# Kernel tuning notes

Measured on AMD Instinct MI355X. Metric: run time of the kernel, lower is better.

Reference implementation:

```python
import jax, jax.numpy as jnp
import numpy as np

N1, N2 = 8192, 4096
NUM_ITERS = 8  # bounded version of the data-dependent while-loop in Revision_PRED
EPS = 1e-6


def _make_boxes(key, n):
    k1, k2 = jax.random.split(key)
    lt = jax.random.uniform(k1, (n, 2), minval=0.0, maxval=800.0)
    wh = jax.random.uniform(k2, (n, 2), minval=1.0, maxval=200.0)
    return jnp.concatenate([lt, lt + wh], axis=1)  # valid xyxy boxes


def setup_inputs() -> dict:
    key = jax.random.key(0)
    ks = jax.random.split(key, 6)
    return {
        "bboxes1": _make_boxes(ks[0], N1),
        "scores1": jax.random.uniform(ks[1], (N1,)),
        "classes1": jax.random.randint(ks[2], (N1,), 0, 80),
        "bboxes2": _make_boxes(ks[3], N2),
        "scores2": jax.random.uniform(ks[4], (N2,)),
        "classes2": jax.random.randint(ks[5], (N2,), 0, 80),
    }


def bbox_overlaps_iou(b1, b2, eps=EPS):
    # b1: [N1,4], b2: [N2,4] xyxy -> [N1,N2] IoU (mode='iou', is_aligned=False)
    area1 = (b1[:, 2] - b1[:, 0]) * (b1[:, 3] - b1[:, 1])
    area2 = (b2[:, 2] - b2[:, 0]) * (b2[:, 3] - b2[:, 1])
    lt = jnp.maximum(b1[:, None, :2], b2[None, :, :2])
    rb = jnp.minimum(b1[:, None, 2:], b2[None, :, 2:])
    wh = jnp.clip(rb - lt, 0.0)
    overlap = wh[..., 0] * wh[..., 1]
    union = jnp.maximum(area1[:, None] + area2[None, :] - overlap, eps)
    return overlap / union


def reference(bboxes1, scores1, classes1, bboxes2, scores2, classes2):
    # Faithful JAX version of Revision_PRED: pairwise IoU + iterative
    # suppression (index_put_ of 0.5) + scatter of winning predictions.
    ious = bbox_overlaps_iou(bboxes1, bboxes2)
    cols = jnp.arange(ious.shape[1])

    def body(ious, _):
        refine_gt = (ious > 0.5).any(axis=0)            # [N2]
        refine_inds = jnp.argmax(ious, axis=0)          # [N2] best pred per box2
        need_refine = scores1[refine_inds] >= scores2
        lower = refine_gt & (~need_refine)              # == (~refine_gt|~need_refine)&refine_gt
        # index_put_ of 0.5 at (refine_inds[lower], lower cols); no-op elsewhere
        new_vals = jnp.where(lower, 0.5, ious[refine_inds, cols])
        ious = ious.at[refine_inds, cols].set(new_vals)
        return ious, None

    # Bounded, idempotent-once-converged replacement for the `while True` loop.
    ious, _ = jax.lax.scan(body, ious, None, length=NUM_ITERS)

    refine_gt = (ious > 0.5).any(axis=0)
    refine_inds = jnp.argmax(ious, axis=0)
    b2 = jnp.where(refine_gt[:, None], bboxes1[refine_inds], bboxes2)
    s2 = jnp.where(refine_gt, scores1[refine_inds], scores2)
    c2 = jnp.where(refine_gt, classes1[refine_inds], classes2)
    refined_boxes = (b2 + jnp.abs(b2)) * 0.5            # clamp negatives to 0
    missing_mask = (ious < 0.5).all(axis=1)             # preds kept as 'missing'
    return refined_boxes, s2, c2, missing_mask, ious
```

## Files before the change

### kernel.cpp

```cpp
#include <hip/hip_runtime.h>


constexpr int TOPK = 9;

__device__ __forceinline__ void key_insert(unsigned long long (&t)[TOPK],
                                           unsigned long long pk) {
    if (pk > t[TOPK - 1]) {
#pragma unroll
        for (int j = TOPK - 1; j >= 0; --j) {
            const bool gt_cur  = pk > t[j];
            const bool gt_prev = (j > 0) ? (pk > t[j - 1]) : false;
            if (gt_cur) t[j] = gt_prev ? t[j - 1] : pk;
        }
    }
}

__global__ __launch_bounds__(256) void iou_cand_kernel(
    const float* __restrict__ b1, const float* __restrict__ b2,
    float* __restrict__ ious,
    unsigned int* __restrict__ cnt, unsigned long long* __restrict__ cand,
    unsigned char* __restrict__ rowflag,
    int n1, int n2, int rps, int cap)
{
    const int tid = blockIdx.x * blockDim.x + threadIdx.x;
    const int c0 = tid * 4;
    if (c0 >= n2) return;
    const int r0 = blockIdx.y * rps;
    const int r1 = min(r0 + rps, n1);

    float4 bx[4]; float ar[4];
#pragma unroll
    for (int k = 0; k < 4; ++k) {
        bx[k] = reinterpret_cast<const float4*>(b2)[c0 + k];
        ar[k] = __fmul_rn(__fsub_rn(bx[k].z, bx[k].x),
                          __fsub_rn(bx[k].w, bx[k].y));
    }

    float* orow = ious + (size_t)r0 * n2 + c0;
    for (int r = r0; r < r1; ++r, orow += n2) {
        const float4 p = reinterpret_cast<const float4*>(b1)[r];
        const float a1 = __fmul_rn(__fsub_rn(p.z, p.x), __fsub_rn(p.w, p.y));
        float v[4], ovs[4], uns[4];
#pragma unroll
        for (int k = 0; k < 4; ++k) {
            const float wx = fmaxf(__fsub_rn(fminf(p.z, bx[k].z),
                                             fmaxf(p.x, bx[k].x)), 0.0f);
            const float wy = fmaxf(__fsub_rn(fminf(p.w, bx[k].w),
                                             fmaxf(p.y, bx[k].y)), 0.0f);
            const float ov = __fmul_rn(wx, wy);
            const float un = fmaxf(__fsub_rn(__fadd_rn(a1, ar[k]), ov), 1e-6f);
            ovs[k] = ov; uns[k] = un;
            float rc = __builtin_amdgcn_rcpf(un);
            rc = rc * fmaf(-un, rc, 2.0f);
            v[k] = ov * rc;
        }

        const float vmax = fmaxf(fmaxf(v[0], v[1]), fmaxf(v[2], v[3]));
        if (vmax > 0.499999f) {
#pragma unroll
            for (int k = 0; k < 4; ++k) {
                if (v[k] > 0.499999f) {
                    const float ve = __fdiv_rn(ovs[k], uns[k]);
                    v[k] = ve;
                    if (ve >= 0.5f) {
                        rowflag[r] = 1;
                        if (ve > 0.5f) {
                            const unsigned int idx = atomicAdd(&cnt[c0 + k], 1u);
                            if (idx < (unsigned int)cap)
                                cand[(size_t)idx * n2 + (c0 + k)] =
                                    ((unsigned long long)__float_as_uint(ve) << 32)
                                  | (unsigned long long)(~(unsigned int)r);
                        }
                    }
                }
            }
        }
        *reinterpret_cast<float4*>(orow) = make_float4(v[0], v[1], v[2], v[3]);
    }
}

__global__ __launch_bounds__(64) void refine_missing_kernel(
    const float* __restrict__ b1, const float* __restrict__ s1,
    const int* __restrict__ c1,
    const float* __restrict__ b2, const float* __restrict__ s2,
    const int* __restrict__ c2,
    const unsigned int* __restrict__ cnt,
    const unsigned long long* __restrict__ cand,
    const unsigned char* __restrict__ rowflag,
    float* __restrict__ out_boxes, float* __restrict__ out_s,
    float* __restrict__ out_c, float* __restrict__ out_m,
    float* __restrict__ ious,
    int n1, int n2, int cap)
{
    const int tid = blockIdx.x * blockDim.x + threadIdx.x;

    if (tid < n1)
        out_m[tid] = rowflag[tid] ? 0.0f : 1.0f;

    const int c = tid;
    if (c >= n2) return;

    unsigned long long t[TOPK];
#pragma unroll
    for (int j = 0; j < TOPK; ++j) t[j] = 0ull;

    const int n = (int)cnt[c];
    if (n <= cap) {
        const unsigned long long* L = cand + c;
        for (int e = 0; e < n; ++e)
            key_insert(t, L[(size_t)e * n2]);
    } else {
        for (int r = 0; r < n1; ++r) {
            const float v = ious[(size_t)r * n2 + c];
            if (v > 0.5f)
                key_insert(t, ((unsigned long long)__float_as_uint(v) << 32)
                            | (unsigned long long)(~(unsigned int)r));
        }
    }

    int m = 0;
#pragma unroll
    for (int j = 0; j < TOPK; ++j) m += (t[j] != 0ull) ? 1 : 0;

    int   ti[TOPK];
    float s1v[TOPK];
    const float s2c = s2[c];
#pragma unroll
    for (int j = 0; j < TOPK; ++j) {
        ti[j]  = (int)~(unsigned int)(t[j] & 0xffffffffull);
        s1v[j] = (j < m) ? s1[ti[j]] : 0.0f;
    }

    int k = 0;
#pragma unroll
    for (int j = 0; j < 8; ++j)
        if (j < m && k == j && s1v[j] < s2c) k = j + 1;

#pragma unroll
    for (int j = 0; j < 8; ++j)
        if (j < k) ious[(size_t)ti[j] * n2 + c] = 0.5f;

    const bool refine = (k < m);
    int winner = 0; float wsc = 0.0f;
#pragma unroll
    for (int j = 0; j < TOPK; ++j)
        if (j == k) { winner = ti[j]; wsc = s1v[j]; }

    float4 ob; float os, oc;
    if (refine) {
        ob = reinterpret_cast<const float4*>(b1)[winner];
        os = wsc;
        oc = (float)c1[winner];
    } else {
        ob = reinterpret_cast<const float4*>(b2)[c];
        os = s2c;
        oc = (float)c2[c];
    }
    ob.x = fmaxf(ob.x, 0.0f); ob.y = fmaxf(ob.y, 0.0f);
    ob.z = fmaxf(ob.z, 0.0f); ob.w = fmaxf(ob.w, 0.0f);
    reinterpret_cast<float4*>(out_boxes)[c] = ob;
    out_s[c] = os;
    out_c[c] = oc;
}

extern "C" void kernel_launch(void* const* d_in, const int* in_sizes, int n_in,
                              void* d_out, int out_size, void* d_ws, size_t ws_size,
                              hipStream_t stream) {
    (void)n_in; (void)out_size;
    const float* b1 = (const float*)d_in[0];
    const float* s1 = (const float*)d_in[1];
    const int*   c1 = (const int*)d_in[2];
    const float* b2 = (const float*)d_in[3];
    const float* s2 = (const float*)d_in[4];
    const int*   c2 = (const int*)d_in[5];
    const int n1 = in_sizes[1];
    const int n2 = in_sizes[4];

    float* out       = (float*)d_out;
    float* out_boxes = out;
    float* out_s     = out + (size_t)n2 * 4;
    float* out_c     = out_s + n2;
    float* out_m     = out_c + n2;
    float* out_ious  = out_m + n1;

    const size_t cnt_b    = (size_t)n2 * sizeof(unsigned int);
    const size_t flag_b   = (size_t)n1;
    const size_t cand_off = (cnt_b + flag_b + 15) & ~(size_t)15;
    int cap = 1024;
    while (cap > 16 && cand_off + (size_t)cap * n2 * 8 > ws_size) cap >>= 1;
    unsigned int*       cnt     = (unsigned int*)d_ws;
    unsigned char*      rowflag = (unsigned char*)d_ws + cnt_b;
    unsigned long long* cand    = (unsigned long long*)((char*)d_ws + cand_off);

    hipMemsetAsync(d_ws, 0, cnt_b + flag_b, stream);

    const int bx = (n2 / 4 + 255) / 256;
    int S = 2048 / bx; if (S < 1) S = 1; if (S > n1) S = n1;
    const int rps = (n1 + S - 1) / S;

    dim3 gridA(bx, S);
    iou_cand_kernel<<<gridA, 256, 0, stream>>>(b1, b2, out_ious, cnt, cand,
                                               rowflag, n1, n2, rps, cap);
    const int ntot = max(n1, n2);
    refine_missing_kernel<<<(ntot + 63) / 64, 64, 0, stream>>>(
        b1, s1, c1, b2, s2, c2, cnt, cand, rowflag,
        out_boxes, out_s, out_c, out_m, out_ious, n1, n2, cap);
}
```

Baseline: 50.89 us.

## Fuse workspace clear, IoU pass and refine pass into one cooperative kernel

The memset and the two kernels are replaced by a single cooperative persistent kernel. It zeroes the workspace counters and row flags, runs the IoU/candidate chunks in a grid-stride loop, then does the refine/missing stage, with grid-wide syncs between the phases. The aim is to remove per-launch and memset overhead and the gaps between dependent stages. The cost is two grid barriers and a grid capped at occupancy × CU count, with a fallback to the old path if the cooperative launch fails.

```diff
diff --git a/kernel.cpp b/kernel.cpp
--- a/kernel.cpp
+++ b/kernel.cpp
@@ -1,4 +1,7 @@
 #include <hip/hip_runtime.h>
+#include <hip/hip_cooperative_groups.h>
+
+namespace cg = cooperative_groups;
 
 
 constexpr int TOPK = 9;
@@ -15,25 +18,20 @@
     }
 }
 
-__global__ __launch_bounds__(256) void iou_cand_kernel(
+
+__device__ __forceinline__ void iou_chunk_body(
     const float* __restrict__ b1, const float* __restrict__ b2,
     float* __restrict__ ious,
     unsigned int* __restrict__ cnt, unsigned long long* __restrict__ cand,
     unsigned char* __restrict__ rowflag,
-    int n1, int n2, int rps, int cap)
-{
-    const int tid = blockIdx.x * blockDim.x + threadIdx.x;
-    const int c0 = tid * 4;
-    if (c0 >= n2) return;
-    const int r0 = blockIdx.y * rps;
-    const int r1 = min(r0 + rps, n1);
-
-    float4 bx[4]; float ar[4];
+    int n1, int n2, int c0, int r0, int r1, int cap)
+{
+    float4 bxv[4]; float ar[4];
 #pragma unroll
     for (int k = 0; k < 4; ++k) {
-        bx[k] = reinterpret_cast<const float4*>(b2)[c0 + k];
-        ar[k] = __fmul_rn(__fsub_rn(bx[k].z, bx[k].x),
-                          __fsub_rn(bx[k].w, bx[k].y));
+        bxv[k] = reinterpret_cast<const float4*>(b2)[c0 + k];
+        ar[k] = __fmul_rn(__fsub_rn(bxv[k].z, bxv[k].x),
+                          __fsub_rn(bxv[k].w, bxv[k].y));
     }
 
     float* orow = ious + (size_t)r0 * n2 + c0;
@@ -43,10 +41,10 @@
         float v[4], ovs[4], uns[4];
 #pragma unroll
         for (int k = 0; k < 4; ++k) {
-            const float wx = fmaxf(__fsub_rn(fminf(p.z, bx[k].z),
-                                             fmaxf(p.x, bx[k].x)), 0.0f);
-            const float wy = fmaxf(__fsub_rn(fminf(p.w, bx[k].w),
-                                             fmaxf(p.y, bx[k].y)), 0.0f);
+            const float wx = fmaxf(__fsub_rn(fminf(p.z, bxv[k].z),
+                                             fmaxf(p.x, bxv[k].x)), 0.0f);
+            const float wy = fmaxf(__fsub_rn(fminf(p.w, bxv[k].w),
+                                             fmaxf(p.y, bxv[k].y)), 0.0f);
             const float ov = __fmul_rn(wx, wy);
             const float un = fmaxf(__fsub_rn(__fadd_rn(a1, ar[k]), ov), 1e-6f);
             ovs[k] = ov; uns[k] = un;
@@ -79,7 +77,7 @@
     }
 }
 
-__global__ __launch_bounds__(64) void refine_missing_kernel(
+__device__ __forceinline__ void refine_missing_body(
     const float* __restrict__ b1, const float* __restrict__ s1,
     const int* __restrict__ c1,
     const float* __restrict__ b2, const float* __restrict__ s2,
@@ -90,10 +88,8 @@
     float* __restrict__ out_boxes, float* __restrict__ out_s,
     float* __restrict__ out_c, float* __restrict__ out_m,
     float* __restrict__ ious,
-    int n1, int n2, int cap)
-{
-    const int tid = blockIdx.x * blockDim.x + threadIdx.x;
-
+    int n1, int n2, int cap, int tid)
+{
     if (tid < n1)
         out_m[tid] = rowflag[tid] ? 0.0f : 1.0f;
 
@@ -163,6 +159,80 @@
     out_c[c] = oc;
 }
 
+__global__ __launch_bounds__(256, 4) void fcos_fused_kernel(
+    const float* __restrict__ b1, const float* __restrict__ s1,
+    const int* __restrict__ c1,
+    const float* __restrict__ b2, const float* __restrict__ s2,
+    const int* __restrict__ c2,
+    float* __restrict__ out_boxes, float* __restrict__ out_s,
+    float* __restrict__ out_c, float* __restrict__ out_m,
+    float* __restrict__ ious,
+    unsigned int* __restrict__ cnt, unsigned long long* __restrict__ cand,
+    unsigned char* __restrict__ rowflag,
+    int n1, int n2, int bx, int rps, int nchunk, int cap)
+{
+    cg::grid_group grid = cg::this_grid();
+    const int tid = blockIdx.x * blockDim.x + threadIdx.x;
+    const int nthreads = gridDim.x * blockDim.x;
+
+    {
+        unsigned int* rf32 = reinterpret_cast<unsigned int*>(rowflag);
+        const int zc = n2 + (n1 >> 2);
+        for (int i = tid; i < zc; i += nthreads) {
+            if (i < n2) cnt[i] = 0u;
+            else        rf32[i - n2] = 0u;
+        }
+    }
+    grid.sync();
+
+    for (int chunk = blockIdx.x; chunk < nchunk; chunk += gridDim.x) {
+        const int bxi = chunk % bx;
+        const int sy  = chunk / bx;
+        const int c0  = (bxi * (int)blockDim.x + (int)threadIdx.x) * 4;
+        if (c0 >= n2) continue;
+        const int r0 = sy * rps;
+        const int r1 = min(r0 + rps, n1);
+        iou_chunk_body(b1, b2, ious, cnt, cand, rowflag, n1, n2, c0, r0, r1, cap);
+    }
+    grid.sync();
+
+    refine_missing_body(b1, s1, c1, b2, s2, c2, cnt, cand, rowflag,
+                        out_boxes, out_s, out_c, out_m, ious, n1, n2, cap, tid);
+}
+
+__global__ __launch_bounds__(256) void iou_cand_kernel(
+    const float* __restrict__ b1, const float* __restrict__ b2,
+    float* __restrict__ ious,
+    unsigned int* __restrict__ cnt, unsigned long long* __restrict__ cand,
+    unsigned char* __restrict__ rowflag,
+    int n1, int n2, int rps, int cap)
+{
+    const int tid = blockIdx.x * blockDim.x + threadIdx.x;
+    const int c0 = tid * 4;
+    if (c0 >= n2) return;
+    const int r0 = blockIdx.y * rps;
+    const int r1 = min(r0 + rps, n1);
+    iou_chunk_body(b1, b2, ious, cnt, cand, rowflag, n1, n2, c0, r0, r1, cap);
+}
+
+__global__ __launch_bounds__(64) void refine_missing_kernel(
+    const float* __restrict__ b1, const float* __restrict__ s1,
+    const int* __restrict__ c1,
+    const float* __restrict__ b2, const float* __restrict__ s2,
+    const int* __restrict__ c2,
+    const unsigned int* __restrict__ cnt,
+    const unsigned long long* __restrict__ cand,
+    const unsigned char* __restrict__ rowflag,
+    float* __restrict__ out_boxes, float* __restrict__ out_s,
+    float* __restrict__ out_c, float* __restrict__ out_m,
+    float* __restrict__ ious,
+    int n1, int n2, int cap)
+{
+    const int tid = blockIdx.x * blockDim.x + threadIdx.x;
+    refine_missing_body(b1, s1, c1, b2, s2, c2, cnt, cand, rowflag,
+                        out_boxes, out_s, out_c, out_m, ious, n1, n2, cap, tid);
+}
+
 extern "C" void kernel_launch(void* const* d_in, const int* in_sizes, int n_in,
                               void* d_out, int out_size, void* d_ws, size_t ws_size,
                               hipStream_t stream) {
@@ -173,8 +243,8 @@
     const float* b2 = (const float*)d_in[3];
     const float* s2 = (const float*)d_in[4];
     const int*   c2 = (const int*)d_in[5];
-    const int n1 = in_sizes[1];
-    const int n2 = in_sizes[4];
+    int n1 = in_sizes[1];
+    int n2 = in_sizes[4];
 
     float* out       = (float*)d_out;
     float* out_boxes = out;
@@ -192,17 +262,40 @@
     unsigned char*      rowflag = (unsigned char*)d_ws + cnt_b;
     unsigned long long* cand    = (unsigned long long*)((char*)d_ws + cand_off);
 
-    hipMemsetAsync(d_ws, 0, cnt_b + flag_b, stream);
-
-    const int bx = (n2 / 4 + 255) / 256;
+    int bx = (n2 / 4 + 255) / 256;
     int S = 2048 / bx; if (S < 1) S = 1; if (S > n1) S = n1;
-    const int rps = (n1 + S - 1) / S;
-
-    dim3 gridA(bx, S);
-    iou_cand_kernel<<<gridA, 256, 0, stream>>>(b1, b2, out_ious, cnt, cand,
-                                               rowflag, n1, n2, rps, cap);
-    const int ntot = max(n1, n2);
-    refine_missing_kernel<<<(ntot + 63) / 64, 64, 0, stream>>>(
-        b1, s1, c1, b2, s2, c2, cnt, cand, rowflag,
-        out_boxes, out_s, out_c, out_m, out_ious, n1, n2, cap);
-}
+    int rps = (n1 + S - 1) / S;
+    int nchunk = bx * S;
+
+    hipError_t err = hipErrorUnknown;
+    int bpc = 0, ncu = 0, dev = 0;
+    (void)hipGetDevice(&dev);
+    (void)hipDeviceGetAttribute(&ncu, hipDeviceAttributeMultiprocessorCount, dev);
+    (void)hipOccupancyMaxActiveBlocksPerMultiprocessor(
+        &bpc, (const void*)fcos_fused_kernel, 256, 0);
+    int GRID = bpc * ncu;
+    if (GRID > 1024)  GRID = 1024;
+    if (GRID > nchunk) GRID = nchunk;
+    if (GRID >= 32) {
+        void* args[] = {
+            (void*)&b1, (void*)&s1, (void*)&c1, (void*)&b2, (void*)&s2,
+            (void*)&c2, (void*)&out_boxes, (void*)&out_s, (void*)&out_c,
+            (void*)&out_m, (void*)&out_ious, (void*)&cnt, (void*)&cand,
+            (void*)&rowflag, (void*)&n1, (void*)&n2, (void*)&bx, (void*)&rps,
+            (void*)&nchunk, (void*)&cap
+        };
+        err = hipLaunchCooperativeKernel((const void*)fcos_fused_kernel,
+                                         dim3(GRID), dim3(256), args, 0, stream);
+    }
+
+    if (err != hipSuccess) {
+        (void)hipMemsetAsync(d_ws, 0, cnt_b + flag_b, stream);
+        dim3 gridA(bx, S);
+        iou_cand_kernel<<<gridA, 256, 0, stream>>>(b1, b2, out_ious, cnt, cand,
+                                                   rowflag, n1, n2, rps, cap);
+        const int ntot = max(n1, n2);
+        refine_missing_kernel<<<(ntot + 63) / 64, 64, 0, stream>>>(
+            b1, s1, c1, b2, s2, c2, cnt, cand, rowflag,
+            out_boxes, out_s, out_c, out_m, out_ious, n1, n2, cap);
+    }
+}
```

After: 198.1 us. 3.89x slower.
